# Performance work log

Hardware: AMD Instinct MI355X
Metric: run time of the kernel (lower is better)

## Reference

```python
import jax, jax.numpy as jnp
import numpy as np

N, E, B = 25600, 307200, 256
H, D, F0, K = 256, 16, 7, 6
GNN_OUT, TDA_IN, TDA_OUT, MEG_IN, MEG_OUT = 192, 32, 128, 16, 64
FUSION = GNN_OUT + TDA_OUT + MEG_OUT  # 384
MID = FUSION // 2  # 192


def _ln(x, g, b, eps=1e-5):
    m = x.mean(-1, keepdims=True)
    v = x.var(-1, keepdims=True)
    return (x - m) * jax.lax.rsqrt(v + eps) * g + b


def _ntn(x, pos, neg):
    return jnp.nan_to_num(x, nan=0.0, posinf=pos, neginf=neg)


def setup_inputs():
    key = jax.random.key(0)
    ks = iter(jax.random.split(key, 80))
    p = lambda *s: 0.05 * jax.random.normal(next(ks), s, jnp.float32)
    inp = {
        "x": jax.random.normal(next(ks), (N, F0), jnp.float32),
        "edge_attr": jax.random.uniform(next(ks), (E, D), dtype=jnp.float32),
        "tda": jax.random.normal(next(ks), (B, TDA_IN), jnp.float32),
        "megnet": jax.random.normal(next(ks), (B, MEG_IN), jnp.float32),
        "edge_index": jax.random.randint(next(ks), (2, E), 0, N),
        "batch": jnp.repeat(jnp.arange(B), N // B),
        # GNN encoder
        "gin_W": p(F0, H), "gin_b": jnp.zeros(H),
        "conv_Wf": p(6, 2 * H + D, H), "conv_bf": jnp.zeros((6, H)),
        "conv_Ws": p(6, 2 * H + D, H), "conv_bs": jnp.zeros((6, H)),
        "gln_g": jnp.ones((6, H)), "gln_b": jnp.zeros((6, H)),
        "gout_W": p(H, GNN_OUT), "gout_b": jnp.zeros(GNN_OUT),
        # TDA projector 32->256->256->128
        "t1_W": p(TDA_IN, 2 * TDA_OUT), "t1_b": jnp.zeros(2 * TDA_OUT),
        "tln1_g": jnp.ones(2 * TDA_OUT), "tln1_b": jnp.zeros(2 * TDA_OUT),
        "t2_W": p(2 * TDA_OUT, 2 * TDA_OUT), "t2_b": jnp.zeros(2 * TDA_OUT),
        "tln2_g": jnp.ones(2 * TDA_OUT), "tln2_b": jnp.zeros(2 * TDA_OUT),
        "t3_W": p(2 * TDA_OUT, TDA_OUT), "t3_b": jnp.zeros(TDA_OUT),
        # MEGNet projector 16->128->128->64
        "m1_W": p(MEG_IN, 2 * MEG_OUT), "m1_b": jnp.zeros(2 * MEG_OUT),
        "mln1_g": jnp.ones(2 * MEG_OUT), "mln1_b": jnp.zeros(2 * MEG_OUT),
        "m2_W": p(2 * MEG_OUT, 2 * MEG_OUT), "m2_b": jnp.zeros(2 * MEG_OUT),
        "mln2_g": jnp.ones(2 * MEG_OUT), "mln2_b": jnp.zeros(2 * MEG_OUT),
        "m3_W": p(2 * MEG_OUT, MEG_OUT), "m3_b": jnp.zeros(MEG_OUT),
        # fusion LN
        "fln_g": jnp.ones(FUSION), "fln_b": jnp.zeros(FUSION),
        # CPPN gate 384->48->24->6
        "g1_W": p(FUSION, K * 8), "g1_b": jnp.zeros(K * 8),
        "hln_g": jnp.ones(K * 8), "hln_b": jnp.zeros(K * 8),
        "g2_W": p(K * 8, K * 4), "g2_b": jnp.zeros(K * 4),
        "g3_W": p(K * 4, K), "g3_b": jnp.zeros(K),
        # CPPN poly branches stacked over K
        "plin_W": p(K, FUSION), "plin_b": jnp.zeros(K),
        "pq1_W": p(K, FUSION, MID), "pq1_b": jnp.zeros((K, MID)),
        "pq2_W": p(K, MID), "pq2_b": jnp.zeros(K),
        "pc1_W": p(K, FUSION, MID // 2), "pc1_b": jnp.zeros((K, MID // 2)),
        "pc2_W": p(K, MID // 2), "pc2_b": jnp.zeros(K),
    }
    return inp


def _forward(x, edge_attr, tda, megnet, edge_index, batch,
             gin_W, gin_b, conv_Wf, conv_bf, conv_Ws, conv_bs, gln_g, gln_b, gout_W, gout_b,
             t1_W, t1_b, tln1_g, tln1_b, t2_W, t2_b, tln2_g, tln2_b, t3_W, t3_b,
             m1_W, m1_b, mln1_g, mln1_b, m2_W, m2_b, mln2_g, mln2_b, m3_W, m3_b,
             fln_g, fln_b,
             g1_W, g1_b, hln_g, hln_b, g2_W, g2_b, g3_W, g3_b,
             plin_W, plin_b, pq1_W, pq1_b, pq2_W, pq2_b, pc1_W, pc1_b, pc2_W, pc2_b):
    silu = jax.nn.silu
    tda = _ntn(tda, 3.0, -3.0)
    megnet = _ntn(megnet, 3.0, -3.0)
    x = _ntn(x, 3.0, -3.0)
    ea = _ntn(edge_attr, 1.0, 0.0)
    src, dst = edge_index[0], edge_index[1]

    h = silu(x @ gin_W + gin_b)  # [N, H]
    for i in range(6):
        # CGConv message: z_ij = [x_i, x_j, e_ij]; sigmoid(z Wf) * softplus(z Ws); sum-agg + root
        z = jnp.concatenate([h[dst], h[src], ea], axis=-1)  # [E, 2H+D]
        msg = jax.nn.sigmoid(z @ conv_Wf[i] + conv_bf[i]) * jax.nn.softplus(z @ conv_Ws[i] + conv_bs[i])
        conv = h + jax.ops.segment_sum(msg, dst, num_segments=N)
        h = _ln(silu(conv) + h, gln_g[i], gln_b[i])
    cnt = jax.ops.segment_sum(jnp.ones((N, 1), h.dtype), batch, num_segments=B)
    pooled = jax.ops.segment_sum(h, batch, num_segments=B) / jnp.maximum(cnt, 1.0)
    z_gnn = jnp.nan_to_num(pooled @ gout_W + gout_b)  # [B, 192]

    # --- projectors ---
    a = _ln(silu(tda @ t1_W + t1_b), tln1_g, tln1_b)
    a = _ln(silu(a @ t2_W + t2_b), tln2_g, tln2_b)
    z_tda = jnp.nan_to_num(a @ t3_W + t3_b)  # [B, 128]
    m = _ln(silu(megnet @ m1_W + m1_b), mln1_g, mln1_b)
    m = _ln(silu(m @ m2_W + m2_b), mln2_g, mln2_b)
    z_meg = jnp.nan_to_num(m @ m3_W + m3_b)  # [B, 64]

    z = _ln(jnp.concatenate([z_gnn, z_tda, z_meg], axis=-1), fln_g, fln_b)  # [B, 384]

    # --- CPPN mixture head ---
    g = _ln(silu(z @ g1_W + g1_b), hln_g, hln_b)
    g = silu(g @ g2_W + g2_b)
    gates = jax.nn.softmax(g @ g3_W + g3_b, axis=-1)  # [B, K]
    lin = jnp.einsum('bd,kd->bk', z, plin_W) + plin_b
    hq = silu(jnp.einsum('bd,kdm->bkm', z, pq1_W) + pq1_b)  # [B, K, 192]
    q = jnp.einsum('bkm,km->bk', hq, pq2_W) + pq2_b
    hc = silu(jnp.einsum('bd,kdm->bkm', z, pc1_W) + pc1_b) ** 2  # [B, K, 96]
    c = jnp.einsum('bkm,km->bk', hc, pc2_W) + pc2_b
    y = (gates * (lin + q + c)).sum(-1)  # [B]
    return y, z


def reference(x, edge_attr, tda, megnet, edge_index, batch,
              gin_W, gin_b, conv_Wf, conv_bf, conv_Ws, conv_bs, gln_g, gln_b, gout_W, gout_b,
              t1_W, t1_b, tln1_g, tln1_b, t2_W, t2_b, tln2_g, tln2_b, t3_W, t3_b,
              m1_W, m1_b, mln1_g, mln1_b, m2_W, m2_b, mln2_g, mln2_b, m3_W, m3_b,
              fln_g, fln_b,
              g1_W, g1_b, hln_g, hln_b, g2_W, g2_b, g3_W, g3_b,
              plin_W, plin_b, pq1_W, pq1_b, pq2_W, pq2_b, pc1_W, pc1_b, pc2_W, pc2_b):
    return _forward(x, edge_attr, tda, megnet, edge_index, batch,
                    gin_W, gin_b, conv_Wf, conv_bf, conv_Ws, conv_bs, gln_g, gln_b, gout_W, gout_b,
                    t1_W, t1_b, tln1_g, tln1_b, t2_W, t2_b, tln2_g, tln2_b, t3_W, t3_b,
                    m1_W, m1_b, mln1_g, mln1_b, m2_W, m2_b, mln2_g, mln2_b, m3_W, m3_b,
                    fln_g, fln_b,
                    g1_W, g1_b, hln_g, hln_b, g2_W, g2_b, g3_W, g3_b,
                    plin_W, plin_b, pq1_W, pq1_b, pq2_W, pq2_b, pc1_W, pc1_b, pc2_W, pc2_b)
```

## Files before the change

kernel.cpp:

```cpp
#include <hip/hip_runtime.h>
#include <hip/hip_bf16.h>
#include <cmath>

#define NN 25600
#define NE 307200
#define NB 256
#define HD 256

typedef __attribute__((ext_vector_type(8))) short short8;
typedef __attribute__((ext_vector_type(4))) float f32x4;
typedef __attribute__((ext_vector_type(2))) float f32x2;

__device__ __forceinline__ float ntn_f(float v, float pos, float neg) {
  if (isnan(v)) return 0.f;
  if (isinf(v)) return v > 0.f ? pos : neg;
  return v;
}
__device__ __forceinline__ float ntn_def(float v) {
  if (isnan(v)) return 0.f;
  if (isinf(v)) return v > 0.f ? 3.4028234663852886e38f : -3.4028234663852886e38f;
  return v;
}
__device__ __forceinline__ float sigmoid_f(float x) { return 1.f / (1.f + __expf(-x)); }
__device__ __forceinline__ float silu_f(float x) { return x * sigmoid_f(x); }
__device__ __forceinline__ float softplus_f(float x) {
  return fmaxf(x, 0.f) + __logf(1.f + __expf(-fabsf(x)));
}
__device__ __forceinline__ unsigned short f2bf(float f) {
  unsigned int u = __float_as_uint(f);
  u += 0x7fffu + ((u >> 16) & 1u);
  return (unsigned short)(u >> 16);
}
__device__ __forceinline__ f32x2 bfpair(unsigned int u) {
  f32x2 r;
  r.x = __uint_as_float(u << 16);
  r.y = __uint_as_float(u & 0xffff0000u);
  return r;
}

template <int NW>
__device__ __forceinline__ float blockSum(float v, float* sred) {
  int lane = threadIdx.x & 63, w = threadIdx.x >> 6;
#pragma unroll
  for (int o = 32; o; o >>= 1) v += __shfl_xor(v, o);
  __syncthreads();
  if (lane == 0) sred[w] = v;
  __syncthreads();
  float r = 0.f;
#pragma unroll
  for (int i = 0; i < NW; ++i) r += sred[i];
  return r;
}

__global__ void k_hist(const int* __restrict__ dst, int* __restrict__ counts, int E) {
  int e = blockIdx.x * 256 + threadIdx.x;
  if (e < E) atomicAdd(&counts[dst[e]], 1);
}

__global__ __launch_bounds__(1024) void k_scan(const int* __restrict__ counts,
                                               int* __restrict__ offs, int n) {
  __shared__ int sd[1024];
  __shared__ int run;
  int tid = threadIdx.x;
  if (tid == 0) run = 0;
  __syncthreads();
  for (int base = 0; base < n; base += 1024) {
    int i = base + tid;
    int v = (i < n) ? counts[i] : 0;
    sd[tid] = v;
    __syncthreads();
    int acc = v;
    for (int off = 1; off < 1024; off <<= 1) {
      int t = (tid >= off) ? sd[tid - off] : 0;
      __syncthreads();
      acc += t;
      sd[tid] = acc;
      __syncthreads();
    }
    int r = run;
    if (i < n) offs[i] = r + acc - v;
    __syncthreads();
    if (tid == 1023) run = r + sd[1023];
    __syncthreads();
  }
  if (threadIdx.x == 0) offs[n] = run;
}

__global__ void k_scatter(const int* __restrict__ dst, const int* __restrict__ offs,
                          int* __restrict__ cursor, int* __restrict__ eidx, int E) {
  int e = blockIdx.x * 256 + threadIdx.x;
  if (e < E) {
    int d = dst[e];
    int p = offs[d] + atomicAdd(&cursor[d], 1);
    eidx[p] = e;
  }
}

__global__ void k_srcperm(const int* __restrict__ eidx, const int* __restrict__ srcArr,
                          int* __restrict__ srcs, int E) {
  int i = blockIdx.x * 256 + threadIdx.x;
  if (i < E) srcs[i] = srcArr[eidx[i]];
}

__global__ void k_eaperm(const int* __restrict__ eidx, const float* __restrict__ ea,
                         float* __restrict__ eacsr, int E) {
  int gid = blockIdx.x * 256 + threadIdx.x;
  if (gid < E * 16) {
    int ii = gid >> 4, k = gid & 15;
    eacsr[gid] = ea[(size_t)eidx[ii] * 16 + k];
  }
}

__global__ void k_pack(const float* __restrict__ conv_Wf, const float* __restrict__ conv_Ws,
                       unsigned short* __restrict__ w4t) {
  int layer = blockIdx.y;
  int gid = blockIdx.x * 256 + threadIdx.x;
  int k = gid & 255;
  int c = gid >> 8;
  int j = c & 255;
  int tbl = c >> 8;
  const float* W = (tbl < 2) ? conv_Wf : conv_Ws;
  int krow = (tbl & 1) ? 256 + k : k;
  float v = W[((size_t)layer * 528 + krow) * 256 + j];
  w4t[((size_t)layer * 1024 + c) * 256 + k] = f2bf(v);
}

__global__ void k_gin(const float* __restrict__ x, const float* __restrict__ W,
                      const float* __restrict__ bias, float* __restrict__ h,
                      unsigned short* __restrict__ hbf) {
  int n = blockIdx.x, j = threadIdx.x;
  float xv[7];
#pragma unroll
  for (int k = 0; k < 7; ++k) xv[k] = ntn_f(x[n * 7 + k], 3.f, -3.f);
  float acc = bias[j];
#pragma unroll
  for (int k = 0; k < 7; ++k) acc += xv[k] * W[k * 256 + j];
  float o = silu_f(acc);
  h[(size_t)n * 256 + j] = o;
  hbf[(size_t)n * 256 + j] = f2bf(o);
}

__global__ __launch_bounds__(256) void k_gemm_bf16(
    const unsigned short* __restrict__ Abf,
    const unsigned short* __restrict__ w4t,
    const float* __restrict__ bf, const float* __restrict__ bs,
    unsigned short* __restrict__ Pout) {
  __shared__ unsigned short As[128 * 56];
  __shared__ unsigned short Bs[128 * 56];
  int tid = threadIdx.x;
  int lane = tid & 63, w = tid >> 6;
  int wr = w >> 1, wc = w & 1;
  int m0 = blockIdx.x * 128, n0 = blockIdx.y * 128;
  int l15 = lane & 15, l4 = lane >> 4;
  f32x4 acc[4][4];
#pragma unroll
  for (int i = 0; i < 4; ++i)
#pragma unroll
    for (int j = 0; j < 4; ++j) acc[i][j] = (f32x4)0.f;
  for (int kt = 0; kt < 8; ++kt) {
    int k0 = kt * 32;
    if (kt) __syncthreads();
#pragma unroll
    for (int c = 0; c < 2; ++c) {
      int chunk = tid + c * 256;
      int row = chunk >> 2, q = chunk & 3;
      *(uint4*)&As[row * 56 + q * 8] =
          *(const uint4*)&Abf[(size_t)(m0 + row) * 256 + k0 + q * 8];
      *(uint4*)&Bs[row * 56 + q * 8] =
          *(const uint4*)&w4t[(size_t)(n0 + row) * 256 + k0 + q * 8];
    }
    __syncthreads();
    short8 a[4], b[4];
#pragma unroll
    for (int f = 0; f < 4; ++f) {
      a[f] = *(const short8*)&As[(wr * 64 + f * 16 + l15) * 56 + l4 * 8];
      b[f] = *(const short8*)&Bs[(wc * 64 + f * 16 + l15) * 56 + l4 * 8];
    }
#pragma unroll
    for (int i = 0; i < 4; ++i)
#pragma unroll
      for (int j = 0; j < 4; ++j)
        acc[i][j] = __builtin_amdgcn_mfma_f32_16x16x32_bf16(a[i], b[j], acc[i][j], 0, 0, 0);
  }
#pragma unroll
  for (int j = 0; j < 4; ++j) {
    int gcol = n0 + wc * 64 + j * 16 + l15;
    float bias = (gcol < 256) ? bf[gcol] : (gcol >= 512 && gcol < 768) ? bs[gcol - 512] : 0.f;
#pragma unroll
    for (int i = 0; i < 4; ++i) {
#pragma unroll
      for (int r = 0; r < 4; ++r) {
        int grow = m0 + wr * 64 + i * 16 + l4 * 4 + r;
        Pout[(size_t)grow * 1024 + gcol] = f2bf(acc[i][j][r] + bias);
      }
    }
  }
}

__global__ __launch_bounds__(256, 1) void k_edge(
    const float* __restrict__ h, const unsigned short* __restrict__ P,
    const float* __restrict__ eacsr,
    const int* __restrict__ srcs, const int* __restrict__ offs,
    const float* __restrict__ WfE, const float* __restrict__ WsE,
    const float* __restrict__ lng, const float* __restrict__ lnb,
    float* __restrict__ hout, unsigned short* __restrict__ hbfout) {
  int lane = threadIdx.x & 63;
  int n = blockIdx.x * 4 + (threadIdx.x >> 6);
  f32x2 wf2[16][2], ws2[16][2];
#pragma unroll
  for (int k = 0; k < 16; ++k) {
    float4 t = *(const float4*)(WfE + k * 256 + lane * 4);
    wf2[k][0].x = t.x; wf2[k][0].y = t.y; wf2[k][1].x = t.z; wf2[k][1].y = t.w;
    float4 u = *(const float4*)(WsE + k * 256 + lane * 4);
    ws2[k][0].x = u.x; ws2[k][0].y = u.y; ws2[k][1].x = u.z; ws2[k][1].y = u.w;
  }
  float4 g4 = *(const float4*)(lng + lane * 4);
  float4 b4 = *(const float4*)(lnb + lane * 4);

  const unsigned short* Pn = P + (size_t)n * 1024;
  uint2 ud0 = *(const uint2*)(Pn + lane * 4);
  uint2 ud1 = *(const uint2*)(Pn + 512 + lane * 4);
  f32x2 pfd0 = bfpair(ud0.x), pfd1 = bfpair(ud0.y);
  f32x2 psd0 = bfpair(ud1.x), psd1 = bfpair(ud1.y);
  float4 hn4 = *(const float4*)(h + (size_t)n * 256 + lane * 4);
  float acc[4] = {0.f, 0.f, 0.f, 0.f};
  int e0 = __builtin_amdgcn_readfirstlane(offs[n]);
  int e1 = __builtin_amdgcn_readfirstlane(offs[n + 1]);

  for (int ii = e0; ii < e1; ++ii) {
    int s = srcs[ii];
    const unsigned short* Ps = P + (size_t)s * 1024;
    uint2 uf = *(const uint2*)(Ps + 256 + lane * 4);
    uint2 us = *(const uint2*)(Ps + 768 + lane * 4);
    float carr[16];
    const float4* ea4 = (const float4*)(eacsr + ((size_t)ii << 4));
    *(float4*)&carr[0] = ea4[0];
    *(float4*)&carr[4] = ea4[1];
    *(float4*)&carr[8] = ea4[2];
    *(float4*)&carr[12] = ea4[3];
    f32x2 af0 = pfd0, af1 = pfd1, as0 = psd0, as1 = psd1;
#pragma unroll
    for (int k = 0; k < 16; ++k) {
      float c = carr[k];
      af0 += c * wf2[k][0]; af1 += c * wf2[k][1];
      as0 += c * ws2[k][0]; as1 += c * ws2[k][1];
    }
    af0 += bfpair(uf.x); af1 += bfpair(uf.y);
    as0 += bfpair(us.x); as1 += bfpair(us.y);
    acc[0] += sigmoid_f(af0.x) * softplus_f(as0.x);
    acc[1] += sigmoid_f(af0.y) * softplus_f(as0.y);
    acc[2] += sigmoid_f(af1.x) * softplus_f(as1.x);
    acc[3] += sigmoid_f(af1.y) * softplus_f(as1.y);
  }
  float hv[4] = {hn4.x, hn4.y, hn4.z, hn4.w};
  float t[4], s1 = 0.f, s2 = 0.f;
#pragma unroll
  for (int q = 0; q < 4; ++q) {
    float cv = hv[q] + acc[q];
    t[q] = silu_f(cv) + hv[q];
    s1 += t[q];
    s2 += t[q] * t[q];
  }
#pragma unroll
  for (int o = 32; o; o >>= 1) {
    s1 += __shfl_xor(s1, o);
    s2 += __shfl_xor(s2, o);
  }
  float mean = s1 * (1.f / 256.f);
  float var = s2 * (1.f / 256.f) - mean * mean;
  float inv = rsqrtf(var + 1e-5f);
  float gg[4] = {g4.x, g4.y, g4.z, g4.w};
  float bb[4] = {b4.x, b4.y, b4.z, b4.w};
  float o0 = (t[0] - mean) * inv * gg[0] + bb[0];
  float o1 = (t[1] - mean) * inv * gg[1] + bb[1];
  float o2 = (t[2] - mean) * inv * gg[2] + bb[2];
  float o3 = (t[3] - mean) * inv * gg[3] + bb[3];
  float4 o4; o4.x = o0; o4.y = o1; o4.z = o2; o4.w = o3;
  *(float4*)(hout + (size_t)n * 256 + lane * 4) = o4;
  uint2 pk;
  pk.x = (unsigned int)f2bf(o0) | ((unsigned int)f2bf(o1) << 16);
  pk.y = (unsigned int)f2bf(o2) | ((unsigned int)f2bf(o3) << 16);
  *(uint2*)(hbfout + (size_t)n * 256 + lane * 4) = pk;
}

__global__ __launch_bounds__(256) void k_pool2(const float* __restrict__ h,
                                               float* __restrict__ pooled) {
  int b = blockIdx.x, j = threadIdx.x;
  const float* hp = h + (size_t)b * 100 * 256 + j;
  float s = 0.f;
  for (int i = 0; i < 100; ++i) s += hp[(size_t)i * 256];
  pooled[b * 256 + j] = s * 0.01f;
}

__global__ void k_zgnn(const float* __restrict__ pooled,
                       const float* __restrict__ W, const float* __restrict__ bias,
                       float* __restrict__ zf) {
  int b = blockIdx.x, j = threadIdx.x;
  float acc = bias[j];
  for (int k = 0; k < 256; ++k) acc += pooled[b * 256 + k] * W[k * 192 + j];
  zf[b * 384 + j] = ntn_def(acc);
}

__global__ __launch_bounds__(256) void k_tda(const float* __restrict__ tda,
    const float* __restrict__ W1, const float* __restrict__ b1,
    const float* __restrict__ g1, const float* __restrict__ bb1,
    const float* __restrict__ W2, const float* __restrict__ b2,
    const float* __restrict__ g2, const float* __restrict__ bb2,
    const float* __restrict__ W3, const float* __restrict__ b3, float* __restrict__ zf) {
  __shared__ float sin_[32];
  __shared__ float sa[256];
  __shared__ float sred[4];
  int b = blockIdx.x, tid = threadIdx.x;
  if (tid < 32) sin_[tid] = ntn_f(tda[b * 32 + tid], 3.f, -3.f);
  __syncthreads();
  float v = b1[tid];
#pragma unroll
  for (int k = 0; k < 32; ++k) v += sin_[k] * W1[k * 256 + tid];
  v = silu_f(v);
  float s1 = blockSum<4>(v, sred);
  float s2 = blockSum<4>(v * v, sred);
  float mean = s1 * (1.f / 256.f), var = s2 * (1.f / 256.f) - mean * mean;
  float inv = rsqrtf(var + 1e-5f);
  v = (v - mean) * inv * g1[tid] + bb1[tid];
  sa[tid] = v;
  __syncthreads();
  float v2 = b2[tid];
  for (int k = 0; k < 256; ++k) v2 += sa[k] * W2[k * 256 + tid];
  v2 = silu_f(v2);
  s1 = blockSum<4>(v2, sred);
  s2 = blockSum<4>(v2 * v2, sred);
  mean = s1 * (1.f / 256.f); var = s2 * (1.f / 256.f) - mean * mean;
  inv = rsqrtf(var + 1e-5f);
  v2 = (v2 - mean) * inv * g2[tid] + bb2[tid];
  __syncthreads();
  sa[tid] = v2;
  __syncthreads();
  if (tid < 128) {
    float o = b3[tid];
    for (int k = 0; k < 256; ++k) o += sa[k] * W3[k * 128 + tid];
    zf[b * 384 + 192 + tid] = ntn_def(o);
  }
}

__global__ __launch_bounds__(128) void k_meg(const float* __restrict__ mg,
    const float* __restrict__ W1, const float* __restrict__ b1,
    const float* __restrict__ g1, const float* __restrict__ bb1,
    const float* __restrict__ W2, const float* __restrict__ b2,
    const float* __restrict__ g2, const float* __restrict__ bb2,
    const float* __restrict__ W3, const float* __restrict__ b3, float* __restrict__ zf) {
  __shared__ float sin_[16];
  __shared__ float sa[128];
  __shared__ float sred[2];
  int b = blockIdx.x, tid = threadIdx.x;
  if (tid < 16) sin_[tid] = ntn_f(mg[b * 16 + tid], 3.f, -3.f);
  __syncthreads();
  float v = b1[tid];
#pragma unroll
  for (int k = 0; k < 16; ++k) v += sin_[k] * W1[k * 128 + tid];
  v = silu_f(v);
  float s1 = blockSum<2>(v, sred);
  float s2 = blockSum<2>(v * v, sred);
  float mean = s1 * (1.f / 128.f), var = s2 * (1.f / 128.f) - mean * mean;
  float inv = rsqrtf(var + 1e-5f);
  v = (v - mean) * inv * g1[tid] + bb1[tid];
  sa[tid] = v;
  __syncthreads();
  float v2 = b2[tid];
  for (int k = 0; k < 128; ++k) v2 += sa[k] * W2[k * 128 + tid];
  v2 = silu_f(v2);
  s1 = blockSum<2>(v2, sred);
  s2 = blockSum<2>(v2 * v2, sred);
  mean = s1 * (1.f / 128.f); var = s2 * (1.f / 128.f) - mean * mean;
  inv = rsqrtf(var + 1e-5f);
  v2 = (v2 - mean) * inv * g2[tid] + bb2[tid];
  __syncthreads();
  sa[tid] = v2;
  __syncthreads();
  if (tid < 64) {
    float o = b3[tid];
    for (int k = 0; k < 128; ++k) o += sa[k] * W3[k * 64 + tid];
    zf[b * 384 + 320 + tid] = ntn_def(o);
  }
}

__global__ __launch_bounds__(384) void k_cppn(const float* __restrict__ zf,
    const float* __restrict__ flng, const float* __restrict__ flnb,
    const float* __restrict__ g1W, const float* __restrict__ g1b,
    const float* __restrict__ hg, const float* __restrict__ hb,
    const float* __restrict__ g2W, const float* __restrict__ g2b,
    const float* __restrict__ g3W, const float* __restrict__ g3b,
    const float* __restrict__ plW, const float* __restrict__ plb,
    const float* __restrict__ pq1W, const float* __restrict__ pq1b,
    const float* __restrict__ pq2W, const float* __restrict__ pq2b,
    const float* __restrict__ pc1W, const float* __restrict__ pc1b,
    const float* __restrict__ pc2W, const float* __restrict__ pc2b,
    float* __restrict__ zout, float* __restrict__ y) {
  __shared__ float sz[384];
  __shared__ float sred[6];
  __shared__ float sg[48];
  __shared__ float s24[24];
  __shared__ float gates[6];
  __shared__ float lin[6];
  __shared__ float qv[6], cvv[6];
  __shared__ float mn48, iv48;
  __shared__ float prodq[1152];
  __shared__ float prodc[576];
  int b = blockIdx.x, tid = threadIdx.x;
  int lane = tid & 63, wv = tid >> 6;

  float v = zf[(size_t)b * 384 + tid];
  float s1 = blockSum<6>(v, sred);
  float s2 = blockSum<6>(v * v, sred);
  float mean = s1 * (1.f / 384.f), var = s2 * (1.f / 384.f) - mean * mean;
  float inv = rsqrtf(var + 1e-5f);
  float zv = (v - mean) * inv * flng[tid] + flnb[tid];
  sz[tid] = zv;
  zout[(size_t)b * 384 + tid] = zv;
  __syncthreads();

  {
    int j = tid >> 3, p = tid & 7;
    float a = 0.f;
    for (int d = p; d < 384; d += 8) a += sz[d] * g1W[d * 48 + j];
    a += __shfl_xor(a, 1);
    a += __shfl_xor(a, 2);
    a += __shfl_xor(a, 4);
    if (p == 0) sg[j] = silu_f(a + g1b[j]);
  }
  __syncthreads();
  if (tid < 64) {
    float x = (tid < 48) ? sg[tid] : 0.f;
    float t1 = x, t2 = x * x;
#pragma unroll
    for (int o = 32; o; o >>= 1) {
      t1 += __shfl_xor(t1, o);
      t2 += __shfl_xor(t2, o);
    }
    if (tid == 0) {
      mn48 = t1 * (1.f / 48.f);
      float vr = t2 * (1.f / 48.f) - mn48 * mn48;
      iv48 = rsqrtf(vr + 1e-5f);
    }
  }
  __syncthreads();
  if (tid < 48) sg[tid] = (sg[tid] - mn48) * iv48 * hg[tid] + hb[tid];
  __syncthreads();
  {
    int j = tid >> 4, p = tid & 15;
    int d0 = p * 3;
    float a = sg[d0] * g2W[d0 * 24 + j] + sg[d0 + 1] * g2W[(d0 + 1) * 24 + j] +
              sg[d0 + 2] * g2W[(d0 + 2) * 24 + j];
    a += __shfl_xor(a, 1);
    a += __shfl_xor(a, 2);
    a += __shfl_xor(a, 4);
    a += __shfl_xor(a, 8);
    if (p == 0) s24[j] = silu_f(a + g2b[j]);
  }
  __syncthreads();
  if (tid < 6) {
    float a = g3b[tid];
    for (int k = 0; k < 24; ++k) a += s24[k] * g3W[k * 6 + tid];
    gates[tid] = a;
  }
  __syncthreads();
  if (tid == 0) {
    float mx = gates[0];
    for (int i = 1; i < 6; ++i) mx = fmaxf(mx, gates[i]);
    float s = 0.f;
    for (int i = 0; i < 6; ++i) { gates[i] = __expf(gates[i] - mx); s += gates[i]; }
    float rs = 1.f / s;
    for (int i = 0; i < 6; ++i) gates[i] *= rs;
  }
  {
    float p = 0.f;
    for (int d = lane; d < 384; d += 64) p += sz[d] * plW[wv * 384 + d];
#pragma unroll
    for (int o = 32; o; o >>= 1) p += __shfl_xor(p, o);
    if (lane == 0) lin[wv] = p + plb[wv];
  }
  if (tid < 288) {
    int k = tid / 48, m4 = (tid % 48) * 4;
    f32x4 a = (f32x4)0.f;
    const float* Wp = pq1W + (size_t)k * 384 * 192 + m4;
    for (int d = 0; d < 384; ++d) {
      float4 w4 = *(const float4*)(Wp + (size_t)d * 192);
      float zd = sz[d];
      a.x += zd * w4.x; a.y += zd * w4.y; a.z += zd * w4.z; a.w += zd * w4.w;
    }
#pragma unroll
    for (int r = 0; r < 4; ++r) {
      int m = m4 + r;
      prodq[k * 192 + m] = silu_f(a[r] + pq1b[k * 192 + m]) * pq2W[k * 192 + m];
    }
  }
  if (tid < 144) {
    int k = tid / 24, m4 = (tid % 24) * 4;
    f32x4 a = (f32x4)0.f;
    const float* Wp = pc1W + (size_t)k * 384 * 96 + m4;
    for (int d = 0; d < 384; ++d) {
      float4 w4 = *(const float4*)(Wp + (size_t)d * 96);
      float zd = sz[d];
      a.x += zd * w4.x; a.y += zd * w4.y; a.z += zd * w4.z; a.w += zd * w4.w;
    }
#pragma unroll
    for (int r = 0; r < 4; ++r) {
      int m = m4 + r;
      float sl = silu_f(a[r] + pc1b[k * 96 + m]);
      prodc[k * 96 + m] = sl * sl * pc2W[k * 96 + m];
    }
  }
  __syncthreads();
  {
    float s = prodq[wv * 192 + lane] + prodq[wv * 192 + 64 + lane] +
              prodq[wv * 192 + 128 + lane];
#pragma unroll
    for (int o = 32; o; o >>= 1) s += __shfl_xor(s, o);
    if (lane == 0) qv[wv] = s + pq2b[wv];
    float c = prodc[wv * 96 + lane] * 1.f;
    float c2 = (lane < 32) ? prodc[wv * 96 + 64 + lane] : 0.f;
    float sc = c + c2;
#pragma unroll
    for (int o = 32; o; o >>= 1) sc += __shfl_xor(sc, o);
    if (lane == 0) cvv[wv] = sc + pc2b[wv];
  }
  __syncthreads();
  if (tid == 0) {
    float yy = 0.f;
    for (int k = 0; k < 6; ++k) yy += gates[k] * (lin[k] + qv[k] + cvv[k]);
    y[b] = yy;
  }
}

extern "C" void kernel_launch(void* const* d_in, const int* in_sizes, int n_in,
                              void* d_out, int out_size, void* d_ws, size_t ws_size,
                              hipStream_t stream) {
  const float* x         = (const float*)d_in[0];
  const float* edge_attr = (const float*)d_in[1];
  const float* tda       = (const float*)d_in[2];
  const float* megnet    = (const float*)d_in[3];
  const int*   edge_index= (const int*)d_in[4];
  const float* gin_W = (const float*)d_in[6];
  const float* gin_b = (const float*)d_in[7];
  const float* conv_Wf = (const float*)d_in[8];
  const float* conv_bf = (const float*)d_in[9];
  const float* conv_Ws = (const float*)d_in[10];
  const float* conv_bs = (const float*)d_in[11];
  const float* gln_g = (const float*)d_in[12];
  const float* gln_b = (const float*)d_in[13];
  const float* gout_W = (const float*)d_in[14];
  const float* gout_b = (const float*)d_in[15];
  const float* t1_W = (const float*)d_in[16];
  const float* t1_b = (const float*)d_in[17];
  const float* tln1_g = (const float*)d_in[18];
  const float* tln1_b = (const float*)d_in[19];
  const float* t2_W = (const float*)d_in[20];
  const float* t2_b = (const float*)d_in[21];
  const float* tln2_g = (const float*)d_in[22];
  const float* tln2_b = (const float*)d_in[23];
  const float* t3_W = (const float*)d_in[24];
  const float* t3_b = (const float*)d_in[25];
  const float* m1_W = (const float*)d_in[26];
  const float* m1_b = (const float*)d_in[27];
  const float* mln1_g = (const float*)d_in[28];
  const float* mln1_b = (const float*)d_in[29];
  const float* m2_W = (const float*)d_in[30];
  const float* m2_b = (const float*)d_in[31];
  const float* mln2_g = (const float*)d_in[32];
  const float* mln2_b = (const float*)d_in[33];
  const float* m3_W = (const float*)d_in[34];
  const float* m3_b = (const float*)d_in[35];
  const float* fln_g = (const float*)d_in[36];
  const float* fln_b = (const float*)d_in[37];
  const float* g1_W = (const float*)d_in[38];
  const float* g1_b = (const float*)d_in[39];
  const float* hln_g = (const float*)d_in[40];
  const float* hln_b = (const float*)d_in[41];
  const float* g2_W = (const float*)d_in[42];
  const float* g2_b = (const float*)d_in[43];
  const float* g3_W = (const float*)d_in[44];
  const float* g3_b = (const float*)d_in[45];
  const float* plin_W = (const float*)d_in[46];
  const float* plin_b = (const float*)d_in[47];
  const float* pq1_W = (const float*)d_in[48];
  const float* pq1_b = (const float*)d_in[49];
  const float* pq2_W = (const float*)d_in[50];
  const float* pq2_b = (const float*)d_in[51];
  const float* pc1_W = (const float*)d_in[52];
  const float* pc1_b = (const float*)d_in[53];
  const float* pc2_W = (const float*)d_in[54];
  const float* pc2_b = (const float*)d_in[55];

  float* ws = (float*)d_ws;
  float* hA = ws;
  float* hB = hA + (size_t)NN * 256;
  float* pooled = hB + (size_t)NN * 256;
  float* zf = pooled + (size_t)NB * 256;
  float* eacsr = zf + (size_t)NB * 384;
  unsigned short* hbfA = (unsigned short*)(eacsr + (size_t)NE * 16);
  unsigned short* hbfB = hbfA + (size_t)NN * 256;
  unsigned short* Pbf = hbfB + (size_t)NN * 256;
  unsigned short* w4t = Pbf + (size_t)NN * 1024;
  int* counts = (int*)(w4t + (size_t)6 * 1024 * 256);
  int* cursor = counts + NN;
  int* offs = cursor + NN;
  int* eidx = offs + NN + 1;
  int* srcs = eidx + NE;

  const int* srcArr = edge_index;
  const int* dstArr = edge_index + NE;

  hipMemsetAsync(counts, 0, (size_t)2 * NN * sizeof(int), stream);

  k_hist<<<(NE + 255) / 256, 256, 0, stream>>>(dstArr, counts, NE);
  k_scan<<<1, 1024, 0, stream>>>(counts, offs, NN);
  k_scatter<<<(NE + 255) / 256, 256, 0, stream>>>(dstArr, offs, cursor, eidx, NE);
  k_srcperm<<<(NE + 255) / 256, 256, 0, stream>>>(eidx, srcArr, srcs, NE);
  k_eaperm<<<(NE * 16 + 255) / 256, 256, 0, stream>>>(eidx, edge_attr, eacsr, NE);
  k_pack<<<dim3(1024, 6), 256, 0, stream>>>(conv_Wf, conv_Ws, w4t);

  k_gin<<<NN, 256, 0, stream>>>(x, gin_W, gin_b, hA, hbfA);

  float* hcur = hA;          float* hnext = hB;
  unsigned short* bcur = hbfA; unsigned short* bnext = hbfB;
  for (int i = 0; i < 6; ++i) {
    const float* Wf = conv_Wf + (size_t)i * 528 * 256;
    const float* Ws = conv_Ws + (size_t)i * 528 * 256;
    k_gemm_bf16<<<dim3(NN / 128, 8), 256, 0, stream>>>(
        bcur, w4t + (size_t)i * 1024 * 256, conv_bf + i * 256, conv_bs + i * 256, Pbf);
    k_edge<<<NN / 4, 256, 0, stream>>>(hcur, Pbf, eacsr, srcs, offs,
                                       Wf + 512 * 256, Ws + 512 * 256,
                                       gln_g + i * 256, gln_b + i * 256, hnext, bnext);
    float* tf = hcur; hcur = hnext; hnext = tf;
    unsigned short* tb = bcur; bcur = bnext; bnext = tb;
  }

  k_pool2<<<NB, 256, 0, stream>>>(hcur, pooled);
  k_zgnn<<<NB, 192, 0, stream>>>(pooled, gout_W, gout_b, zf);
  k_tda<<<NB, 256, 0, stream>>>(tda, t1_W, t1_b, tln1_g, tln1_b, t2_W, t2_b, tln2_g, tln2_b,
                                t3_W, t3_b, zf);
  k_meg<<<NB, 128, 0, stream>>>(megnet, m1_W, m1_b, mln1_g, mln1_b, m2_W, m2_b, mln2_g, mln2_b,
                                m3_W, m3_b, zf);

  float* yout = (float*)d_out;
  float* zout = yout + NB;
  k_cppn<<<NB, 384, 0, stream>>>(zf, fln_g, fln_b,
                                 g1_W, g1_b, hln_g, hln_b, g2_W, g2_b, g3_W, g3_b,
                                 plin_W, plin_b, pq1_W, pq1_b, pq2_W, pq2_b,
                                 pc1_W, pc1_b, pc2_W, pc2_b, zout, yout);
}
```

Before: 1.387 ms.

## Split each node's edge aggregation across two wavefronts

```diff
diff --git a/kernel.cpp b/kernel.cpp
--- a/kernel.cpp
+++ b/kernel.cpp
@@ -197,90 +197,84 @@
   }
 }
 
-__global__ __launch_bounds__(256, 1) void k_edge(
+__global__ __launch_bounds__(256, 2) void k_edge(
     const float* __restrict__ h, const unsigned short* __restrict__ P,
     const float* __restrict__ eacsr,
     const int* __restrict__ srcs, const int* __restrict__ offs,
     const float* __restrict__ WfE, const float* __restrict__ WsE,
     const float* __restrict__ lng, const float* __restrict__ lnb,
     float* __restrict__ hout, unsigned short* __restrict__ hbfout) {
-  int lane = threadIdx.x & 63;
-  int n = blockIdx.x * 4 + (threadIdx.x >> 6);
-  f32x2 wf2[16][2], ws2[16][2];
+  __shared__ float sr1[4], sr2[4];
+  int tid = threadIdx.x;
+  int lane = tid & 63;
+  int w = tid >> 6;
+  int n = blockIdx.x * 2 + (w >> 1);
+  int half = w & 1;
+  int idx = half * 128 + lane * 2;
+  f32x2 wf2[16], ws2[16];
 #pragma unroll
   for (int k = 0; k < 16; ++k) {
-    float4 t = *(const float4*)(WfE + k * 256 + lane * 4);
-    wf2[k][0].x = t.x; wf2[k][0].y = t.y; wf2[k][1].x = t.z; wf2[k][1].y = t.w;
-    float4 u = *(const float4*)(WsE + k * 256 + lane * 4);
-    ws2[k][0].x = u.x; ws2[k][0].y = u.y; ws2[k][1].x = u.z; ws2[k][1].y = u.w;
-  }
-  float4 g4 = *(const float4*)(lng + lane * 4);
-  float4 b4 = *(const float4*)(lnb + lane * 4);
+    wf2[k] = *(const f32x2*)(WfE + k * 256 + idx);
+    ws2[k] = *(const f32x2*)(WsE + k * 256 + idx);
+  }
+  f32x2 lg = *(const f32x2*)(lng + idx);
+  f32x2 lb = *(const f32x2*)(lnb + idx);
 
   const unsigned short* Pn = P + (size_t)n * 1024;
-  uint2 ud0 = *(const uint2*)(Pn + lane * 4);
-  uint2 ud1 = *(const uint2*)(Pn + 512 + lane * 4);
-  f32x2 pfd0 = bfpair(ud0.x), pfd1 = bfpair(ud0.y);
-  f32x2 psd0 = bfpair(ud1.x), psd1 = bfpair(ud1.y);
-  float4 hn4 = *(const float4*)(h + (size_t)n * 256 + lane * 4);
-  float acc[4] = {0.f, 0.f, 0.f, 0.f};
+  f32x2 pfd = bfpair(*(const unsigned int*)(Pn + idx));
+  f32x2 psd = bfpair(*(const unsigned int*)(Pn + 512 + idx));
+  f32x2 hn = *(const f32x2*)(h + (size_t)n * 256 + idx);
+  f32x2 acc = (f32x2)0.f;
   int e0 = __builtin_amdgcn_readfirstlane(offs[n]);
   int e1 = __builtin_amdgcn_readfirstlane(offs[n + 1]);
 
   for (int ii = e0; ii < e1; ++ii) {
     int s = srcs[ii];
     const unsigned short* Ps = P + (size_t)s * 1024;
-    uint2 uf = *(const uint2*)(Ps + 256 + lane * 4);
-    uint2 us = *(const uint2*)(Ps + 768 + lane * 4);
+    unsigned int uf = *(const unsigned int*)(Ps + 256 + idx);
+    unsigned int us = *(const unsigned int*)(Ps + 768 + idx);
     float carr[16];
     const float4* ea4 = (const float4*)(eacsr + ((size_t)ii << 4));
     *(float4*)&carr[0] = ea4[0];
     *(float4*)&carr[4] = ea4[1];
     *(float4*)&carr[8] = ea4[2];
     *(float4*)&carr[12] = ea4[3];
-    f32x2 af0 = pfd0, af1 = pfd1, as0 = psd0, as1 = psd1;
+    f32x2 af = pfd, as_ = psd;
 #pragma unroll
     for (int k = 0; k < 16; ++k) {
       float c = carr[k];
-      af0 += c * wf2[k][0]; af1 += c * wf2[k][1];
-      as0 += c * ws2[k][0]; as1 += c * ws2[k][1];
-    }
-    af0 += bfpair(uf.x); af1 += bfpair(uf.y);
-    as0 += bfpair(us.x); as1 += bfpair(us.y);
-    acc[0] += sigmoid_f(af0.x) * softplus_f(as0.x);
-    acc[1] += sigmoid_f(af0.y) * softplus_f(as0.y);
-    acc[2] += sigmoid_f(af1.x) * softplus_f(as1.x);
-    acc[3] += sigmoid_f(af1.y) * softplus_f(as1.y);
-  }
-  float hv[4] = {hn4.x, hn4.y, hn4.z, hn4.w};
-  float t[4], s1 = 0.f, s2 = 0.f;
-#pragma unroll
-  for (int q = 0; q < 4; ++q) {
-    float cv = hv[q] + acc[q];
-    t[q] = silu_f(cv) + hv[q];
-    s1 += t[q];
-    s2 += t[q] * t[q];
-  }
+      af += c * wf2[k];
+      as_ += c * ws2[k];
+    }
+    af += bfpair(uf);
+    as_ += bfpair(us);
+    acc.x += sigmoid_f(af.x) * softplus_f(as_.x);
+    acc.y += sigmoid_f(af.y) * softplus_f(as_.y);
+  }
+  float cv0 = hn.x + acc.x;
+  float cv1 = hn.y + acc.y;
+  float t0 = silu_f(cv0) + hn.x;
+  float t1 = silu_f(cv1) + hn.y;
+  float s1 = t0 + t1, s2 = t0 * t0 + t1 * t1;
 #pragma unroll
   for (int o = 32; o; o >>= 1) {
     s1 += __shfl_xor(s1, o);
     s2 += __shfl_xor(s2, o);
   }
-  float mean = s1 * (1.f / 256.f);
-  float var = s2 * (1.f / 256.f) - mean * mean;
+  if (lane == 0) { sr1[w] = s1; sr2[w] = s2; }
+  __syncthreads();
+  int pw = w ^ 1;
+  float S1 = sr1[w] + sr1[pw];
+  float S2 = sr2[w] + sr2[pw];
+  float mean = S1 * (1.f / 256.f);
+  float var = S2 * (1.f / 256.f) - mean * mean;
   float inv = rsqrtf(var + 1e-5f);
-  float gg[4] = {g4.x, g4.y, g4.z, g4.w};
-  float bb[4] = {b4.x, b4.y, b4.z, b4.w};
-  float o0 = (t[0] - mean) * inv * gg[0] + bb[0];
-  float o1 = (t[1] - mean) * inv * gg[1] + bb[1];
-  float o2 = (t[2] - mean) * inv * gg[2] + bb[2];
-  float o3 = (t[3] - mean) * inv * gg[3] + bb[3];
-  float4 o4; o4.x = o0; o4.y = o1; o4.z = o2; o4.w = o3;
-  *(float4*)(hout + (size_t)n * 256 + lane * 4) = o4;
-  uint2 pk;
-  pk.x = (unsigned int)f2bf(o0) | ((unsigned int)f2bf(o1) << 16);
-  pk.y = (unsigned int)f2bf(o2) | ((unsigned int)f2bf(o3) << 16);
-  *(uint2*)(hbfout + (size_t)n * 256 + lane * 4) = pk;
+  float o0 = (t0 - mean) * inv * lg.x + lb.x;
+  float o1 = (t1 - mean) * inv * lg.y + lb.y;
+  f32x2 ov; ov.x = o0; ov.y = o1;
+  *(f32x2*)(hout + (size_t)n * 256 + idx) = ov;
+  unsigned int pk = (unsigned int)f2bf(o0) | ((unsigned int)f2bf(o1) << 16);
+  *(unsigned int*)(hbfout + (size_t)n * 256 + idx) = pk;
 }
 
 __global__ __launch_bounds__(256) void k_pool2(const float* __restrict__ h,
@@ -516,7 +510,7 @@
 #pragma unroll
     for (int o = 32; o; o >>= 1) s += __shfl_xor(s, o);
     if (lane == 0) qv[wv] = s + pq2b[wv];
-    float c = prodc[wv * 96 + lane] * 1.f;
+    float c = prodc[wv * 96 + lane];
     float c2 = (lane < 32) ? prodc[wv * 96 + 64 + lane] : 0.f;
     float sc = c + c2;
 #pragma unroll
@@ -627,7 +621,7 @@
     const float* Ws = conv_Ws + (size_t)i * 528 * 256;
     k_gemm_bf16<<<dim3(NN / 128, 8), 256, 0, stream>>>(
         bcur, w4t + (size_t)i * 1024 * 256, conv_bf + i * 256, conv_bs + i * 256, Pbf);
-    k_edge<<<NN / 4, 256, 0, stream>>>(hcur, Pbf, eacsr, srcs, offs,
+    k_edge<<<NN / 2, 256, 0, stream>>>(hcur, Pbf, eacsr, srcs, offs,
                                        Wf + 512 * 256, Ws + 512 * 256,
                                        gln_g + i * 256, gln_b + i * 256, hnext, bnext);
     float* tf = hcur; hcur = hnext; hnext = tf;
```

Result: no change. 1.361 ms (-1.8%).
